# Optimization experiments

Hardware: AMD Instinct MI355X
Metric: run time of the kernel (lower is better)

The kernel has to match this reference:

```python
import jax, jax.numpy as jnp
import numpy as np


def setup_inputs() -> dict:
    key = jax.random.key(0)
    k1, k2, k3 = jax.random.split(key, 3)
    N, P, C = 4, 1024, 3
    H, W = 128, 128
    # coordinates in pixel space: x in [0, W), y in [0, H)
    coords01 = jax.random.uniform(k1, (N, P, 2), dtype=jnp.float32)
    coordinates = coords01 * jnp.array([W, H], dtype=jnp.float32)
    values = jax.random.normal(k2, (N, P, C), dtype=jnp.float32)
    # sigma in [1.0, 3.0), one std per batch element
    sigma = 1.0 + 2.0 * jax.random.uniform(k3, (N, 1), dtype=jnp.float32)
    return {
        "coordinates": coordinates,
        "values": values,
        "sigma": sigma,
        "height": H,
        "width": W,
    }


def reference(coordinates, values, sigma, height, width):
    # coordinates: [N, P, 2] (x, y); values: [N, P, C]; sigma: [N, 1]
    dt = coordinates.dtype
    ys = jnp.arange(height, dtype=dt)  # [H]
    xs = jnp.arange(width, dtype=dt)   # [W]
    x = coordinates[..., 0]            # [N, P]
    y = coordinates[..., 1]            # [N, P]
    # squared distance from each point to each grid cell: [N, P, H, W]
    dy2 = (ys[None, None, :, None] - y[:, :, None, None]) ** 2  # [N,P,H,1]
    dx2 = (xs[None, None, None, :] - x[:, :, None, None]) ** 2  # [N,P,1,W]
    dist2 = dy2 + dx2                                           # [N,P,H,W]
    inv_two_sigma2 = 0.5 / (sigma ** 2)                         # [N,1]
    weight = jnp.exp(-dist2 * inv_two_sigma2[:, :, None, None])  # [N,P,H,W]
    # scatter-add each point's gaussian-weighted value onto the grid
    out = jnp.einsum('nphw,npc->nchw', weight, values)  # [N,C,H,W]
    return out
```

## Files before the change

### kernel.cpp

```cpp
#include <hip/hip_runtime.h>
#include <hip/hip_bf16.h>


#define BLOCK 256
#define SEGS  8

__device__ __forceinline__ float fast_exp2(float x) {
#if __has_builtin(__builtin_amdgcn_exp2f)
    return __builtin_amdgcn_exp2f(x);
#else
    return exp2f(x);
#endif
}

__global__ __launch_bounds__(BLOCK) void splat2d_lds(
    const float* __restrict__ coords,
    const float* __restrict__ vals,
    const float* __restrict__ sigma,
    const int*   __restrict__ wptr,
    float*       __restrict__ out,
    int P, int pixPerN, int blocksPerN, int nSeg)
{
    const int PS_MAX = 1024;
    __shared__ float4 ptA[PS_MAX / SEGS];
    __shared__ float2 ptB[PS_MAX / SEGS];

    const int W = *wptr;
    int t = blockIdx.x;
    const int seg = t % nSeg;  t /= nSeg;
    const int n   = t / blocksPerN;
    const int blk = t % blocksPerN;

    const float sg = sigma[n];
    const float s  = -1.44269504088896f * 0.5f / (sg * sg);

    const int PS = P / nSeg;
    const int p0 = seg * PS;
    const float* __restrict__ cp = coords + ((size_t)n * P + p0) * 2;
    const float* __restrict__ vp = vals   + ((size_t)n * P + p0) * 3;

    for (int p = threadIdx.x; p < PS; p += BLOCK) {
        const float x  = cp[2 * p + 0];
        const float y  = cp[2 * p + 1];
        const float v0 = vp[3 * p + 0];
        const float v1 = vp[3 * p + 1];
        const float v2 = vp[3 * p + 2];
        const float c  = s * fmaf(x, x, y * y);
        ptA[p] = make_float4(x, y, c, v0);
        ptB[p] = make_float2(v1, v2);
    }
    __syncthreads();

    const int pix = blk * BLOCK + threadIdx.x;
    const int h = pix / W;
    const int w = pix - h * W;
    const float fx = (float)w;
    const float fy = (float)h;
    const float tx = -2.0f * s * fx;
    const float ty = -2.0f * s * fy;
    const float bb = s * fmaf(fx, fx, fy * fy);

    float a0 = 0.f, a1 = 0.f, a2 = 0.f;

#pragma unroll 8
    for (int p = 0; p < PS; ++p) {
        const float4 q = ptA[p];
        const float2 r = ptB[p];
        const float e = fmaf(tx, q.x, fmaf(ty, q.y, bb + q.z));
        const float wgt = fast_exp2(e);
        a0 = fmaf(wgt, q.w, a0);
        a1 = fmaf(wgt, r.x, a1);
        a2 = fmaf(wgt, r.y, a2);
    }

    const size_t base = ((size_t)n * 3) * (size_t)pixPerN + (size_t)pix;
    unsafeAtomicAdd(&out[base],                       a0);
    unsafeAtomicAdd(&out[base + (size_t)pixPerN],     a1);
    unsafeAtomicAdd(&out[base + 2 * (size_t)pixPerN], a2);
}

extern "C" void kernel_launch(void* const* d_in, const int* in_sizes, int n_in,
                              void* d_out, int out_size, void* d_ws, size_t ws_size,
                              hipStream_t stream) {
    const float* coords = (const float*)d_in[0];
    const float* vals   = (const float*)d_in[1];
    const float* sigma  = (const float*)d_in[2];
    const int* wptr = (const int*)d_in[4];

    const int N = in_sizes[2];
    const int P = in_sizes[0] / (2 * N);
    const int C = in_sizes[1] / (N * P);
    const int pixPerN = out_size / (N * C);

    float* out = (float*)d_out;

    const int nSeg = (P % SEGS == 0 && P <= 1024) ? SEGS : 1;
    const int blocksPerN = pixPerN / BLOCK;
    const int grid = N * blocksPerN * nSeg;

    hipMemsetAsync(out, 0, (size_t)out_size * sizeof(float), stream);

    splat2d_lds<<<grid, BLOCK, 0, stream>>>(coords, vals, sigma, wptr,
                                            out, P, pixPerN, blocksPerN, nSeg);
}
```

Before: 75.85 us.

## Add row-per-block splat kernel with precomputed separable y-weights and in-block reduction

Adds a kernel where each 1024-thread block handles one image row. The y-direction Gaussian factor is computed once per point and folded into the values, so the inner loop needs one fewer FMA. The eight point segments are summed in shared memory and written with plain stores, which removes the atomics and the memset. The fast path is gated on a hardcoded 128x128 shape. The grid shrinks to N*H blocks of 1024 threads, and the block now preloads all points into LDS instead of one segment, which adds per-block setup work.

Measured after the change: 74.56 us. Within noise of the previous version (-1.7%).

```diff
diff --git a/kernel.cpp b/kernel.cpp
--- a/kernel.cpp
+++ b/kernel.cpp
@@ -2,8 +2,8 @@
 #include <hip/hip_bf16.h>
 
 
-#define BLOCK 256
-#define SEGS  8
+#define MAINBLOCK 1024
+#define NSEG 8
 
 __device__ __forceinline__ float fast_exp2(float x) {
 #if __has_builtin(__builtin_amdgcn_exp2f)
@@ -13,13 +13,93 @@
 #endif
 }
 
-__global__ __launch_bounds__(BLOCK) void splat2d_lds(
+__global__ __launch_bounds__(MAINBLOCK) void splat2d_row(
     const float* __restrict__ coords,
     const float* __restrict__ vals,
     const float* __restrict__ sigma,
-    const int*   __restrict__ wptr,
     float*       __restrict__ out,
-    int P, int pixPerN, int blocksPerN, int nSeg)
+    int P, int H, int W)
+{
+    __shared__ float4 ptA[1024];
+    __shared__ float  ptB[1024];
+    __shared__ float  red0[MAINBLOCK];
+    __shared__ float  red1[MAINBLOCK];
+    __shared__ float  red2[MAINBLOCK];
+
+    const int n = blockIdx.x / H;
+    const int h = blockIdx.x % H;
+    const int tid = threadIdx.x;
+    const int px  = tid & 127;
+    const int seg = tid >> 7;
+
+    const float sg = sigma[n];
+    const float s  = -1.44269504088896f * 0.5f / (sg * sg);
+    const float fh = (float)h;
+
+    const float* __restrict__ cp = coords + (size_t)n * P * 2;
+    const float* __restrict__ vp = vals   + (size_t)n * P * 3;
+
+    for (int p = tid; p < P; p += MAINBLOCK) {
+        const float x  = cp[2 * p + 0];
+        const float y  = cp[2 * p + 1];
+        const float v0 = vp[3 * p + 0];
+        const float v1 = vp[3 * p + 1];
+        const float v2 = vp[3 * p + 2];
+        const float dy = fh - y;
+        const float rh = fast_exp2(s * dy * dy);
+        ptA[p] = make_float4(-2.0f * s * x,
+                             s * x * x,
+                             rh * v0, rh * v1);
+        ptB[p] = rh * v2;
+    }
+    __syncthreads();
+
+    const float fx  = (float)px;
+    const float bbx = s * fx * fx;
+
+    const int PS = P / NSEG;
+    const int p0 = seg * PS;
+
+    float a0 = 0.f, a1 = 0.f, a2 = 0.f;
+
+#pragma unroll 8
+    for (int i = 0; i < PS; ++i) {
+        const float4 q  = ptA[p0 + i];
+        const float  v2 = ptB[p0 + i];
+        const float  t  = q.y + bbx;
+        const float  e  = fmaf(q.x, fx, t);
+        const float  wg = fast_exp2(e);
+        a0 = fmaf(wg, q.z, a0);
+        a1 = fmaf(wg, q.w, a1);
+        a2 = fmaf(wg, v2, a2);
+    }
+
+    red0[tid] = a0; red1[tid] = a1; red2[tid] = a2;
+    __syncthreads();
+
+    if (tid < 128) {
+        float s0 = 0.f, s1 = 0.f, s2 = 0.f;
+#pragma unroll
+        for (int k = 0; k < NSEG; ++k) {
+            s0 += red0[tid + 128 * k];
+            s1 += red1[tid + 128 * k];
+            s2 += red2[tid + 128 * k];
+        }
+        const size_t hw = (size_t)H * W;
+        const size_t base = ((size_t)n * 3) * hw + (size_t)h * W + tid;
+        out[base]          = s0;
+        out[base + hw]     = s1;
+        out[base + 2 * hw] = s2;
+    }
+}
+
+#define BLOCK 256
+#define SEGS  8
+
+__global__ __launch_bounds__(BLOCK) void splat2d_lds(
+    const float* __restrict__ coords, const float* __restrict__ vals,
+    const float* __restrict__ sigma, const int* __restrict__ wptr,
+    float* __restrict__ out, int P, int pixPerN, int blocksPerN, int nSeg)
 {
     const int PS_MAX = 1024;
     __shared__ float4 ptA[PS_MAX / SEGS];
@@ -42,26 +122,20 @@
     for (int p = threadIdx.x; p < PS; p += BLOCK) {
         const float x  = cp[2 * p + 0];
         const float y  = cp[2 * p + 1];
-        const float v0 = vp[3 * p + 0];
-        const float v1 = vp[3 * p + 1];
-        const float v2 = vp[3 * p + 2];
         const float c  = s * fmaf(x, x, y * y);
-        ptA[p] = make_float4(x, y, c, v0);
-        ptB[p] = make_float2(v1, v2);
+        ptA[p] = make_float4(x, y, c, vp[3 * p + 0]);
+        ptB[p] = make_float2(vp[3 * p + 1], vp[3 * p + 2]);
     }
     __syncthreads();
 
     const int pix = blk * BLOCK + threadIdx.x;
     const int h = pix / W;
     const int w = pix - h * W;
-    const float fx = (float)w;
-    const float fy = (float)h;
-    const float tx = -2.0f * s * fx;
-    const float ty = -2.0f * s * fy;
+    const float fx = (float)w, fy = (float)h;
+    const float tx = -2.0f * s * fx, ty = -2.0f * s * fy;
     const float bb = s * fmaf(fx, fx, fy * fy);
 
     float a0 = 0.f, a1 = 0.f, a2 = 0.f;
-
 #pragma unroll 8
     for (int p = 0; p < PS; ++p) {
         const float4 q = ptA[p];
@@ -85,6 +159,7 @@
     const float* coords = (const float*)d_in[0];
     const float* vals   = (const float*)d_in[1];
     const float* sigma  = (const float*)d_in[2];
+    const int* hptr = (const int*)d_in[3];
     const int* wptr = (const int*)d_in[4];
 
     const int N = in_sizes[2];
@@ -94,12 +169,18 @@
 
     float* out = (float*)d_out;
 
-    const int nSeg = (P % SEGS == 0 && P <= 1024) ? SEGS : 1;
-    const int blocksPerN = pixPerN / BLOCK;
-    const int grid = N * blocksPerN * nSeg;
-
-    hipMemsetAsync(out, 0, (size_t)out_size * sizeof(float), stream);
-
-    splat2d_lds<<<grid, BLOCK, 0, stream>>>(coords, vals, sigma, wptr,
-                                            out, P, pixPerN, blocksPerN, nSeg);
+    if (pixPerN == 16384 && P <= 1024 && (P % NSEG) == 0 && C == 3) {
+        const int H = 128, W = 128;
+        const int grid = N * H;
+        splat2d_row<<<grid, MAINBLOCK, 0, stream>>>(coords, vals, sigma,
+                                                    out, P, H, W);
+        (void)hptr; (void)wptr;
+    } else {
+        const int nSeg = (P % SEGS == 0 && P <= 1024) ? SEGS : 1;
+        const int blocksPerN = pixPerN / BLOCK;
+        const int grid = N * blocksPerN * nSeg;
+        hipMemsetAsync(out, 0, (size_t)out_size * sizeof(float), stream);
+        splat2d_lds<<<grid, BLOCK, 0, stream>>>(coords, vals, sigma, wptr,
+                                                out, P, pixPerN, blocksPerN, nSeg);
+    }
 }
```
